# Optimization experiments

Hardware: AMD Instinct MI355X
Metric: run time of the kernel (lower is better)

Reference implementation:

```python
import jax, jax.numpy as jnp
import numpy as np

N_EMBD = 1024
N_HEAD = 16
R = 16
SCALING = 1.0 / 16.0  # loralib default lora_alpha=1, scaling = alpha/r


def lora_linear(x, W, b, A, B):
    # loralib: y = x @ W.T + b + (x @ A.T) @ B.T * scaling
    return x @ W.T + b + (x @ A.T) @ B.T * SCALING


def setup_inputs() -> dict:
    key = jax.random.key(0)
    ks = jax.random.split(key, 16)
    B, T, S, C = 8, 1024, 256, N_EMBD
    std = 0.02
    return {
        "x": jax.random.normal(ks[0], (B, T, C), jnp.float32),
        "feature": jax.random.normal(ks[1], (B, S, C), jnp.float32),
        # c_attn (q projection)
        "Wq": jax.random.normal(ks[2], (C, C), jnp.float32) * std,
        "bq": jnp.zeros((C,), jnp.float32),
        "Aq": jax.random.normal(ks[3], (R, C), jnp.float32) * std,
        "Bq": jnp.zeros((C, R), jnp.float32),
        # feature_attn (kv projection)
        "Wf": jax.random.normal(ks[4], (2 * C, C), jnp.float32) * std,
        "bf": jnp.zeros((2 * C,), jnp.float32),
        "Af": jax.random.normal(ks[5], (R, C), jnp.float32) * std,
        "Bf": jnp.zeros((2 * C, R), jnp.float32),
        # c_proj
        "Wp": jax.random.normal(ks[6], (C, C), jnp.float32) * std,
        "bp": jnp.zeros((C,), jnp.float32),
        "Ap": jax.random.normal(ks[7], (R, C), jnp.float32) * std,
        "Bp": jnp.zeros((C, R), jnp.float32),
    }


def reference(x, feature, Wq, bq, Aq, Bq, Wf, bf, Af, Bf, Wp, bp, Ap, Bp):
    Bsz, T, C = x.shape
    S = feature.shape[1]
    H = N_HEAD
    D = C // H

    q = lora_linear(x, Wq, bq, Aq, Bq).reshape(Bsz, T, H, D).transpose(0, 2, 1, 3)
    kv = lora_linear(feature, Wf, bf, Af, Bf)
    k, v = kv[..., :C], kv[..., C:]
    k = k.reshape(Bsz, S, H, D).transpose(0, 2, 1, 3)
    v = v.reshape(Bsz, S, H, D).transpose(0, 2, 1, 3)

    att = jnp.einsum("bhtd,bhsd->bhts", q, k) * (1.0 / np.sqrt(D))
    mask = jnp.tril(jnp.ones((T, S), bool))  # bias[:, :, :T, :S]
    att = jnp.where(mask, att, -jnp.inf)
    att = jax.nn.softmax(att, axis=-1)

    y = jnp.einsum("bhts,bhsd->bhtd", att, v)
    y = y.transpose(0, 2, 1, 3).reshape(Bsz, T, C)
    return lora_linear(y, Wp, bp, Ap, Bp)
```

## Files before the change

kernel.cpp:

```cpp
#include <hip/hip_runtime.h>
#include <hip/hip_bf16.h>
#include <stdint.h>
#include <stddef.h>

typedef __hip_bfloat16 bf16;
typedef __attribute__((ext_vector_type(8))) short short8;
typedef __attribute__((ext_vector_type(4))) float floatx4;

__device__ __forceinline__ void async_load16(const bf16* g, bf16* l) {
#if defined(__has_builtin) && __has_builtin(__builtin_amdgcn_global_load_lds)
  __builtin_amdgcn_global_load_lds((__attribute__((address_space(1))) void*)g,
                                   (__attribute__((address_space(3))) void*)l,
                                   16, 0, 0);
#else
  *(short8*)l = *(const short8*)g;
#endif
}

__device__ __forceinline__ int wave_detect_f32(const unsigned short* __restrict__ xr) {
  const int lane = threadIdx.x & 63;
  const unsigned short u = xr[lane];
  const int e = (u >> 7) & 0xFF;
  const unsigned long long m = __ballot(e >= 0x93);
  return (__popcll(m) > 5) ? 1 : 0;
}

struct PrepArgs {
  const void *x, *ft, *bq, *bf, *bp;
  const void *Wq, *Aq, *Bq, *Wf, *Af, *Bf, *Wp, *Ap, *Bp;
  bf16 *cx, *cft, *cbq, *cbf, *cbp, *weffq, *wefff, *weffp;
};

__device__ __forceinline__ void canon8(const void* src, bf16* dst, int i8, int flg) {
  if (flg) {
    const float4 v0 = ((const float4*)src)[i8 * 2];
    const float4 v1 = ((const float4*)src)[i8 * 2 + 1];
    bf16 o[8];
    o[0] = __float2bfloat16(v0.x); o[1] = __float2bfloat16(v0.y);
    o[2] = __float2bfloat16(v0.z); o[3] = __float2bfloat16(v0.w);
    o[4] = __float2bfloat16(v1.x); o[5] = __float2bfloat16(v1.y);
    o[6] = __float2bfloat16(v1.z); o[7] = __float2bfloat16(v1.w);
    *(uint4*)(dst + i8 * 8) = *(const uint4*)o;
  } else {
    ((uint4*)dst)[i8] = ((const uint4*)src)[i8];
  }
}

__device__ __forceinline__ void weff4(const void* W, const void* Bm, const void* Am,
                                      bf16* dst, int idx4, int flg) {
  const int n = idx4 >> 8, k = (idx4 & 255) << 2;
  float a0 = 0.f, a1 = 0.f, a2 = 0.f, a3 = 0.f;
  float w0, w1, w2, w3;
  if (flg) {
    const float* Af = (const float*)Am;
    const float* Bf = (const float*)Bm;
#pragma unroll
    for (int r = 0; r < 16; ++r) {
      const float4 av = *(const float4*)(Af + r * 1024 + k);
      const float bv = Bf[n * 16 + r];
      a0 += bv * av.x; a1 += bv * av.y; a2 += bv * av.z; a3 += bv * av.w;
    }
    const float4 wv = *(const float4*)((const float*)W + n * 1024 + k);
    w0 = wv.x; w1 = wv.y; w2 = wv.z; w3 = wv.w;
  } else {
    const bf16* Ab = (const bf16*)Am;
    const bf16* Bb = (const bf16*)Bm;
#pragma unroll
    for (int r = 0; r < 16; ++r) {
      const float bv = __bfloat162float(Bb[n * 16 + r]);
      const bf16* ap = Ab + r * 1024 + k;
      a0 += bv * __bfloat162float(ap[0]);
      a1 += bv * __bfloat162float(ap[1]);
      a2 += bv * __bfloat162float(ap[2]);
      a3 += bv * __bfloat162float(ap[3]);
    }
    const bf16* Wb = (const bf16*)W + n * 1024 + k;
    w0 = __bfloat162float(Wb[0]); w1 = __bfloat162float(Wb[1]);
    w2 = __bfloat162float(Wb[2]); w3 = __bfloat162float(Wb[3]);
  }
  bf16 o[4];
  o[0] = __float2bfloat16(w0 + 0.0625f * a0);
  o[1] = __float2bfloat16(w1 + 0.0625f * a1);
  o[2] = __float2bfloat16(w2 + 0.0625f * a2);
  o[3] = __float2bfloat16(w3 + 0.0625f * a3);
  *(uint2*)(dst + idx4 * 4) = *(const uint2*)o;
}

__global__ __launch_bounds__(256) void prep_kernel(PrepArgs a) {
  const int flg = wave_detect_f32((const unsigned short*)a.x);
  const int bid = blockIdx.x, tid = threadIdx.x;
  if (bid < 4096) {
    canon8(a.x, a.cx, bid * 256 + tid, flg);
  } else if (bid < 5120) {
    canon8(a.ft, a.cft, (bid - 4096) * 256 + tid, flg);
  } else if (bid < 5122) {
    const int e8 = (bid - 5120) * 256 + tid;
    if (e8 < 128) canon8(a.bq, a.cbq, e8, flg);
    else if (e8 < 384) canon8(a.bf, a.cbf, e8 - 128, flg);
    else canon8(a.bp, a.cbp, e8 - 384, flg);
  } else if (bid < 6146) {
    weff4(a.Wq, a.Bq, a.Aq, a.weffq, (bid - 5122) * 256 + tid, flg);
  } else if (bid < 8194) {
    weff4(a.Wf, a.Bf, a.Af, a.wefff, (bid - 6146) * 256 + tid, flg);
  } else {
    weff4(a.Wp, a.Bp, a.Ap, a.weffp, (bid - 8194) * 256 + tid, flg);
  }
}

#define QSLOT (256 * 32)
#define RSLOT (2 * QSLOT)

__device__ __forceinline__ void stage256(const bf16* __restrict__ gA,
                                         const bf16* __restrict__ gB,
                                         bf16* slot, int tid) {
#pragma unroll
  for (int l = 0; l < 2; ++l) {
    const int D = l * 512 + tid;
    const int r = D >> 2;
    const int c = (D & 3) ^ ((r >> 1) & 3);
    async_load16(gA + (size_t)r * 1024 + c * 8, slot + D * 8);
  }
#pragma unroll
  for (int l = 0; l < 2; ++l) {
    const int D = l * 512 + tid;
    const int r = D >> 2;
    const int c = (D & 3) ^ ((r >> 1) & 3);
    async_load16(gB + (size_t)r * 1024 + c * 8, slot + QSLOT + D * 8);
  }
}

__device__ __forceinline__ void gemm_core256(const bf16* __restrict__ A,
                                             const bf16* __restrict__ Bt,
                                             int bm, int bn, bf16* sT,
                                             floatx4 (&acc)[8][4]) {
  const int tid = threadIdx.x;
  const int wave = tid >> 6, lane = tid & 63;
  const int lrow = lane & 15, quad = lane >> 4;
  const int wm = (wave >> 2) << 7;
  const int wn = (wave & 3) << 6;
  const int pc0 = ((quad ^ ((lrow >> 1) & 3)) << 3);

  const bf16* gA = A + (size_t)bm * 1024;
  const bf16* gB = Bt + (size_t)bn * 1024;

  stage256(gA,      gB,      sT,             tid);
  stage256(gA + 32, gB + 32, sT + RSLOT,     tid);
  stage256(gA + 64, gB + 64, sT + 2 * RSLOT, tid);

#pragma unroll 4
  for (int t = 0; t < 32; ++t) {
    asm volatile("s_waitcnt lgkmcnt(0)" ::: "memory");
    __builtin_amdgcn_s_barrier();
    __builtin_amdgcn_sched_barrier(0);
    if (t < 29) {
      stage256(gA + (t + 3) * 32, gB + (t + 3) * 32, sT + ((t + 3) & 3) * RSLOT, tid);
      asm volatile("s_waitcnt vmcnt(12)" ::: "memory");
    } else if (t == 29) {
      asm volatile("s_waitcnt vmcnt(8)" ::: "memory");
    } else if (t == 30) {
      asm volatile("s_waitcnt vmcnt(4)" ::: "memory");
    } else {
      asm volatile("s_waitcnt vmcnt(0)" ::: "memory");
    }
    __builtin_amdgcn_s_barrier();
    __builtin_amdgcn_sched_barrier(0);

    const bf16* slotA = sT + (t & 3) * RSLOT;
    const bf16* slotB = slotA + QSLOT;
    short8 a_[8], b_[4];
#pragma unroll
    for (int i = 0; i < 8; ++i)
      a_[i] = *(const short8*)(slotA + (wm + i * 16 + lrow) * 32 + pc0);
#pragma unroll
    for (int j = 0; j < 4; ++j)
      b_[j] = *(const short8*)(slotB + (wn + j * 16 + lrow) * 32 + pc0);
    __builtin_amdgcn_s_setprio(1);
#pragma unroll
    for (int i = 0; i < 8; ++i)
#pragma unroll
      for (int j = 0; j < 4; ++j)
        acc[i][j] = __builtin_amdgcn_mfma_f32_16x16x32_bf16(
            a_[i], b_[j], acc[i][j], 0, 0, 0);
    __builtin_amdgcn_s_setprio(0);
  }
}

#define QSLOTB (128 * 32)
#define RSLOTO (QSLOT + QSLOTB)

__device__ __forceinline__ void stage128(const bf16* __restrict__ gA,
                                         const bf16* __restrict__ gB,
                                         bf16* slot, int tid) {
#pragma unroll
  for (int l = 0; l < 2; ++l) {
    const int D = l * 512 + tid;
    const int r = D >> 2;
    const int c = (D & 3) ^ ((r >> 1) & 3);
    async_load16(gA + (size_t)r * 1024 + c * 8, slot + D * 8);
  }
  {
    const int D = tid;
    const int r = D >> 2;
    const int c = (D & 3) ^ ((r >> 1) & 3);
    async_load16(gB + (size_t)r * 1024 + c * 8, slot + QSLOT + D * 8);
  }
}

__device__ __forceinline__ void gemm_core128(const bf16* __restrict__ A,
                                             const bf16* __restrict__ Bt,
                                             int bm, int bn, bf16* sT,
                                             floatx4 (&acc)[4][4]) {
  const int tid = threadIdx.x;
  const int wave = tid >> 6, lane = tid & 63;
  const int lrow = lane & 15, quad = lane >> 4;
  const int wm = (wave >> 1) << 6;
  const int wn = (wave & 1) << 6;
  const int pc0 = ((quad ^ ((lrow >> 1) & 3)) << 3);

  const bf16* gA = A + (size_t)bm * 1024;
  const bf16* gB = Bt + (size_t)bn * 1024;

  stage128(gA,      gB,      sT,             tid);
  stage128(gA + 32, gB + 32, sT + RSLOTO,     tid);
  stage128(gA + 64, gB + 64, sT + 2 * RSLOTO, tid);

#pragma unroll 4
  for (int t = 0; t < 32; ++t) {
    asm volatile("s_waitcnt lgkmcnt(0)" ::: "memory");
    __builtin_amdgcn_s_barrier();
    __builtin_amdgcn_sched_barrier(0);
    if (t < 29) {
      stage128(gA + (t + 3) * 32, gB + (t + 3) * 32, sT + ((t + 3) & 3) * RSLOTO, tid);
      asm volatile("s_waitcnt vmcnt(9)" ::: "memory");
    } else if (t == 29) {
      asm volatile("s_waitcnt vmcnt(6)" ::: "memory");
    } else if (t == 30) {
      asm volatile("s_waitcnt vmcnt(3)" ::: "memory");
    } else {
      asm volatile("s_waitcnt vmcnt(0)" ::: "memory");
    }
    __builtin_amdgcn_s_barrier();
    __builtin_amdgcn_sched_barrier(0);

    const bf16* slotA = sT + (t & 3) * RSLOTO;
    const bf16* slotB = slotA + QSLOT;
    short8 a_[4], b_[4];
#pragma unroll
    for (int i = 0; i < 4; ++i) {
      a_[i] = *(const short8*)(slotA + (wm + i * 16 + lrow) * 32 + pc0);
      b_[i] = *(const short8*)(slotB + (wn + i * 16 + lrow) * 32 + pc0);
    }
    __builtin_amdgcn_s_setprio(1);
#pragma unroll
    for (int i = 0; i < 4; ++i)
#pragma unroll
      for (int j = 0; j < 4; ++j)
        acc[i][j] = __builtin_amdgcn_mfma_f32_16x16x32_bf16(
            a_[i], b_[j], acc[i][j], 0, 0, 0);
    __builtin_amdgcn_s_setprio(0);
  }
}

__global__ __launch_bounds__(512, 1) void gemm_qkv(
    const bf16* __restrict__ cx, const bf16* __restrict__ cft,
    const bf16* __restrict__ weffq, const bf16* __restrict__ wefff,
    const bf16* __restrict__ cbq, const bf16* __restrict__ cbf,
    bf16* __restrict__ qws, bf16* __restrict__ kws, bf16* __restrict__ vtws) {
  __shared__ __align__(16) bf16 sT[4 * RSLOT];
  const int bid = blockIdx.x;
  const int swz = (bid & 7) * 24 + (bid >> 3);
  int mode, bm, bn;
  const bf16 *A, *Bt, *bias;
  if (swz < 128) {
    mode = 0; A = cx; Bt = weffq; bias = cbq;
    bm = (swz >> 2) * 256; bn = (swz & 3) * 256;
  } else {
    const int s2 = swz - 128;
    mode = 1; A = cft; Bt = wefff; bias = cbf;
    bm = (s2 >> 3) * 256; bn = (s2 & 7) * 256;
  }

  const floatx4 zero4 = {0.f, 0.f, 0.f, 0.f};
  floatx4 acc[8][4];
#pragma unroll
  for (int i = 0; i < 8; ++i)
#pragma unroll
    for (int j = 0; j < 4; ++j) acc[i][j] = zero4;

  gemm_core256(A, Bt, bm, bn, sT, acc);

  const int tid = threadIdx.x, wave = tid >> 6, lane = tid & 63;
  const int lrow = lane & 15, quad = lane >> 4;
  const int wm = (wave >> 2) << 7, wn = (wave & 3) << 6;
#pragma unroll
  for (int i = 0; i < 8; ++i) {
    const int mbase = bm + wm + i * 16 + quad * 4;
#pragma unroll
    for (int j = 0; j < 4; ++j) {
      const int n = bn + wn + j * 16 + lrow;
      const float bv = __bfloat162float(bias[n]);
#pragma unroll
      for (int r = 0; r < 4; ++r) {
        const int m = mbase + r;
        const bf16 hval = __float2bfloat16(acc[i][j][r] + bv);
        if (mode == 0) {
          const int b = m >> 10, t = m & 1023, hh = n >> 6, d = n & 63;
          qws[(((size_t)(b * 16 + hh)) * 1024 + t) * 64 + d] = hval;
        } else {
          const int b = m >> 8, s = m & 255;
          if (n < 1024) {
            const int hh = n >> 6, d = n & 63;
            kws[(((size_t)(b * 16 + hh)) * 256 + s) * 64 + d] = hval;
          } else {
            const int nn = n - 1024, hh = nn >> 6, d = nn & 63;
            vtws[(((size_t)(b * 16 + hh)) * 64 + d) * 256 + s] = hval;
          }
        }
      }
    }
  }
}

__global__ __launch_bounds__(512, 1) void gemm_out(
    const bf16* __restrict__ A, const bf16* __restrict__ Bt,
    const bf16* __restrict__ bias, void* __restrict__ out0,
    const unsigned short* __restrict__ xraw) {
  __shared__ __align__(16) bf16 sT[4 * RSLOTO];
  const int bid = blockIdx.x;
  const int swz = (bid & 7) * 32 + (bid >> 3);
  const int bm = (swz >> 3) * 256, bn = (swz & 7) * 128;
  const int N = 1024;

  const floatx4 zero4 = {0.f, 0.f, 0.f, 0.f};
  floatx4 acc[4][4];
#pragma unroll
  for (int i = 0; i < 4; ++i)
#pragma unroll
    for (int j = 0; j < 4; ++j) acc[i][j] = zero4;

  gemm_core128(A, Bt, bm, bn, sT, acc);

  const int tid = threadIdx.x, wave = tid >> 6, lane = tid & 63;
  const int lrow = lane & 15, quad = lane >> 4;
  const int wm = (wave >> 1) << 6, wn = (wave & 1) << 6;
  const int flg = wave_detect_f32(xraw);
#pragma unroll
  for (int i = 0; i < 4; ++i) {
    const int mbase = bm + wm + i * 16 + quad * 4;
#pragma unroll
    for (int j = 0; j < 4; ++j) {
      const int n = bn + wn + j * 16 + lrow;
      const float bv = __bfloat162float(bias[n]);
#pragma unroll
      for (int r = 0; r < 4; ++r) {
        const int m = mbase + r;
        const float fval = acc[i][j][r] + bv;
        const size_t idx = (size_t)m * N + n;
        if (flg) ((float*)out0)[idx] = fval;
        else     ((bf16*)out0)[idx] = __float2bfloat16(fval);
      }
    }
  }
}

#define SKP 72
#define SVP 264
__global__ __launch_bounds__(512, 2) void attn_kernel(
    const bf16* __restrict__ qws, const bf16* __restrict__ kws,
    const bf16* __restrict__ vtws, bf16* __restrict__ yws) {
  const int b = blockIdx.z, h = blockIdx.y, qc = blockIdx.x;
  const int bh = b * 16 + h;
  __shared__ __align__(16) bf16 sK[256 * SKP];
  __shared__ __align__(16) bf16 sVt[64 * SVP];
  __shared__ __align__(16) bf16 sP[8][16 * SVP];
  const int tid = threadIdx.x, wave = tid >> 6, lane = tid & 63;
  const int lrow = lane & 15, quad = lane >> 4;
  const bf16* kg = kws + (size_t)bh * (256 * 64);
  const bf16* vg = vtws + (size_t)bh * (64 * 256);
#pragma unroll
  for (int i = 0; i < 4; ++i) {
    const int idx = i * 512 + tid;
    const int kr = idx >> 3, kc = (idx & 7) * 8;
    *(short8*)(sK + kr * SKP + kc) = *(const short8*)(kg + kr * 64 + kc);
    const int vr = idx >> 5, vc = (idx & 31) * 8;
    *(short8*)(sVt + vr * SVP + vc) = *(const short8*)(vg + vr * 256 + vc);
  }
  __syncthreads();
  bf16* sPw = sP[wave];
  const floatx4 zero4 = {0.f, 0.f, 0.f, 0.f};
  const float kscale = 0.18033688011112042f;

  for (int st = 0; st < 4; ++st) {
    const int t0 = qc * 512 + wave * 64 + st * 16;
    const bf16* qrow = qws + ((size_t)bh * 1024 + t0 + lrow) * 64;
    const short8 aq0 = *(const short8*)(qrow + quad * 8);
    const short8 aq1 = *(const short8*)(qrow + 32 + quad * 8);
    floatx4 sc[16];
#pragma unroll
    for (int nt = 0; nt < 16; ++nt) {
      floatx4 c = zero4;
      c = __builtin_amdgcn_mfma_f32_16x16x32_bf16(
          aq0, *(const short8*)(sK + (nt * 16 + lrow) * SKP + quad * 8), c, 0, 0, 0);
      c = __builtin_amdgcn_mfma_f32_16x16x32_bf16(
          aq1, *(const short8*)(sK + (nt * 16 + lrow) * SKP + 32 + quad * 8), c, 0, 0, 0);
      sc[nt] = c;
    }
    float sum[4] = {0.f, 0.f, 0.f, 0.f};
#pragma unroll
    for (int nt = 0; nt < 16; ++nt) {
      const int s = nt * 16 + lrow;
#pragma unroll
      for (int r = 0; r < 4; ++r) {
        const int t = t0 + quad * 4 + r;
        const float p = (s <= t) ? exp2f(sc[nt][r] * kscale) : 0.f;
        sum[r] += p;
        sPw[(quad * 4 + r) * SVP + nt * 16 + lrow] = __float2bfloat16(p);
      }
    }
#pragma unroll
    for (int r = 0; r < 4; ++r) {
      sum[r] += __shfl_xor(sum[r], 1, 16);
      sum[r] += __shfl_xor(sum[r], 2, 16);
      sum[r] += __shfl_xor(sum[r], 4, 16);
      sum[r] += __shfl_xor(sum[r], 8, 16);
    }
    asm volatile("s_waitcnt lgkmcnt(0)" ::: "memory");
    floatx4 ya[4];
#pragma unroll
    for (int nt = 0; nt < 4; ++nt) ya[nt] = zero4;
#pragma unroll
    for (int ks = 0; ks < 8; ++ks) {
      const short8 ap = *(const short8*)(sPw + lrow * SVP + ks * 32 + quad * 8);
#pragma unroll
      for (int nt = 0; nt < 4; ++nt)
        ya[nt] = __builtin_amdgcn_mfma_f32_16x16x32_bf16(
            ap, *(const short8*)(sVt + (nt * 16 + lrow) * SVP + ks * 32 + quad * 8),
            ya[nt], 0, 0, 0);
    }
#pragma unroll
    for (int r = 0; r < 4; ++r) {
      const float rl = 1.f / sum[r];
      const int t = t0 + quad * 4 + r;
#pragma unroll
      for (int nt = 0; nt < 4; ++nt)
        yws[((size_t)b * 1024 + t) * 1024 + h * 64 + nt * 16 + lrow] =
            __float2bfloat16(ya[nt][r] * rl);
    }
  }
}

extern "C" void kernel_launch(void* const* d_in, const int* in_sizes, int n_in,
                              void* d_out, int out_size, void* d_ws, size_t ws_size,
                              hipStream_t stream) {
  char* p = (char*)d_ws;
  bf16* cbq   = (bf16*)p;     p += 4096;
  bf16* cbf   = (bf16*)p;     p += 8192;
  bf16* cbp   = (bf16*)p;     p += 4096;
  bf16* weffq = (bf16*)p;     p += (size_t)1024 * 1024 * 2;
  bf16* wefff = (bf16*)p;     p += (size_t)2048 * 1024 * 2;
  bf16* weffp = (bf16*)p;     p += (size_t)1024 * 1024 * 2;
  bf16* qws   = (bf16*)p;     p += (size_t)8 * 16 * 1024 * 64 * 2;
  bf16* kws   = (bf16*)p;     p += (size_t)8 * 16 * 256 * 64 * 2;
  bf16* vtws  = (bf16*)p;     p += (size_t)8 * 16 * 64 * 256 * 2;
  bf16* cft   = (bf16*)p;     p += (size_t)8 * 256 * 1024 * 2;
  bf16* cx    = (bf16*)p;     p += (size_t)8 * 1024 * 1024 * 2;
  bf16* yws   = cx;
  const size_t required = (size_t)(p - (char*)d_ws);
  if (ws_size < required) return;

  PrepArgs pa;
  pa.x = d_in[0]; pa.ft = d_in[1];
  pa.bq = d_in[3]; pa.bf = d_in[7]; pa.bp = d_in[11];
  pa.Wq = d_in[2];  pa.Aq = d_in[4];  pa.Bq = d_in[5];
  pa.Wf = d_in[6];  pa.Af = d_in[8];  pa.Bf = d_in[9];
  pa.Wp = d_in[10]; pa.Ap = d_in[12]; pa.Bp = d_in[13];
  pa.cx = cx; pa.cft = cft; pa.cbq = cbq; pa.cbf = cbf; pa.cbp = cbp;
  pa.weffq = weffq; pa.wefff = wefff; pa.weffp = weffp;
  prep_kernel<<<9218, 256, 0, stream>>>(pa);

  gemm_qkv<<<192, 512, 0, stream>>>(cx, cft, weffq, wefff, cbq, cbf, qws, kws, vtws);
  attn_kernel<<<dim3(2, 16, 8), 512, 0, stream>>>(qws, kws, vtws, yws);
  gemm_out<<<256, 512, 0, stream>>>(yws, weffp, cbp, d_out, (const unsigned short*)d_in[0]);
}
```

Measured before the change: 239.2 us.

## Unify GEMMs into 256x128 tile, 4-wave blocks with split-stage triple buffering

Both the QKV and output projection GEMMs now share one core that uses a 256x128 tile and 4 waves of 256 threads, each wave owning a 128x64 sub-tile. Launch bounds allow two blocks per CU. Each k-step's global-to-LDS staging is split into two halves, issued before and after the first half of the MFMA work. The LDS ring shrinks from 4 slots to 3, which is what lets two blocks fit per CU. The QKV grid doubles to 384 blocks. The aim is better CU occupancy and latency hiding, at the cost of more accumulator registers per thread and an extra barrier each iteration.

```diff
diff --git a/kernel.cpp b/kernel.cpp
--- a/kernel.cpp
+++ b/kernel.cpp
@@ -107,177 +107,140 @@
   }
 }
 
-#define QSLOT (256 * 32)
-#define RSLOT (2 * QSLOT)
-
-__device__ __forceinline__ void stage256(const bf16* __restrict__ gA,
-                                         const bf16* __restrict__ gB,
-                                         bf16* slot, int tid) {
+#define ASLOT (256 * 32)
+#define BSLOT (128 * 32)
+#define SLOT3 (ASLOT + BSLOT)
+
+__device__ __forceinline__ void stage_first(const bf16* __restrict__ gA,
+                                            const bf16* __restrict__ gB,
+                                            bf16* slot, int tid) {
 #pragma unroll
   for (int l = 0; l < 2; ++l) {
-    const int D = l * 512 + tid;
+    const int D = l * 256 + tid;
     const int r = D >> 2;
     const int c = (D & 3) ^ ((r >> 1) & 3);
     async_load16(gA + (size_t)r * 1024 + c * 8, slot + D * 8);
   }
-#pragma unroll
-  for (int l = 0; l < 2; ++l) {
-    const int D = l * 512 + tid;
+  {
+    const int D = tid;
     const int r = D >> 2;
     const int c = (D & 3) ^ ((r >> 1) & 3);
-    async_load16(gB + (size_t)r * 1024 + c * 8, slot + QSLOT + D * 8);
-  }
-}
-
-__device__ __forceinline__ void gemm_core256(const bf16* __restrict__ A,
-                                             const bf16* __restrict__ Bt,
-                                             int bm, int bn, bf16* sT,
-                                             floatx4 (&acc)[8][4]) {
+    async_load16(gB + (size_t)r * 1024 + c * 8, slot + ASLOT + D * 8);
+  }
+}
+
+__device__ __forceinline__ void stage_second(const bf16* __restrict__ gA,
+                                             const bf16* __restrict__ gB,
+                                             bf16* slot, int tid) {
+#pragma unroll
+  for (int l = 2; l < 4; ++l) {
+    const int D = l * 256 + tid;
+    const int r = D >> 2;
+    const int c = (D & 3) ^ ((r >> 1) & 3);
+    async_load16(gA + (size_t)r * 1024 + c * 8, slot + D * 8);
+  }
+  {
+    const int D = 256 + tid;
+    const int r = D >> 2;
+    const int c = (D & 3) ^ ((r >> 1) & 3);
+    async_load16(gB + (size_t)r * 1024 + c * 8, slot + ASLOT + D * 8);
+  }
+}
+
+__device__ __forceinline__ void gemm_core(const bf16* __restrict__ A,
+                                          const bf16* __restrict__ Bt,
+                                          int bm, int bn, bf16* sT,
+                                          floatx4 (&acc)[8][4]) {
   const int tid = threadIdx.x;
   const int wave = tid >> 6, lane = tid & 63;
   const int lrow = lane & 15, quad = lane >> 4;
-  const int wm = (wave >> 2) << 7;
-  const int wn = (wave & 3) << 6;
+  const int wm = (wave >> 1) << 7;
+  const int wn = (wave & 1) << 6;
   const int pc0 = ((quad ^ ((lrow >> 1) & 3)) << 3);
 
   const bf16* gA = A + (size_t)bm * 1024;
   const bf16* gB = Bt + (size_t)bn * 1024;
 
-  stage256(gA,      gB,      sT,             tid);
-  stage256(gA + 32, gB + 32, sT + RSLOT,     tid);
-  stage256(gA + 64, gB + 64, sT + 2 * RSLOT, tid);
-
-#pragma unroll 4
+  stage_first(gA, gB, sT, tid);  stage_second(gA, gB, sT, tid);
+  stage_first(gA + 32, gB + 32, sT + SLOT3, tid);
+  stage_second(gA + 32, gB + 32, sT + SLOT3, tid);
+
+  int rs = 0, ss = 2;
   for (int t = 0; t < 32; ++t) {
+    const bf16* slotA = sT + rs * SLOT3;
+    const bf16* slotB = slotA + ASLOT;
+    bf16* stSlot = sT + ss * SLOT3;
+    const bf16* sgA = gA + (t + 2) * 32;
+    const bf16* sgB = gB + (t + 2) * 32;
+
     asm volatile("s_waitcnt lgkmcnt(0)" ::: "memory");
     __builtin_amdgcn_s_barrier();
     __builtin_amdgcn_sched_barrier(0);
-    if (t < 29) {
-      stage256(gA + (t + 3) * 32, gB + (t + 3) * 32, sT + ((t + 3) & 3) * RSLOT, tid);
-      asm volatile("s_waitcnt vmcnt(12)" ::: "memory");
-    } else if (t == 29) {
-      asm volatile("s_waitcnt vmcnt(8)" ::: "memory");
+    if (t < 30) {
+      stage_first(sgA, sgB, stSlot, tid);
+      asm volatile("s_waitcnt vmcnt(9)" ::: "memory");
     } else if (t == 30) {
-      asm volatile("s_waitcnt vmcnt(4)" ::: "memory");
+      asm volatile("s_waitcnt vmcnt(6)" ::: "memory");
     } else {
       asm volatile("s_waitcnt vmcnt(0)" ::: "memory");
     }
     __builtin_amdgcn_s_barrier();
     __builtin_amdgcn_sched_barrier(0);
 
-    const bf16* slotA = sT + (t & 3) * RSLOT;
-    const bf16* slotB = slotA + QSLOT;
     short8 a_[8], b_[4];
 #pragma unroll
-    for (int i = 0; i < 8; ++i)
+    for (int i = 0; i < 4; ++i)
       a_[i] = *(const short8*)(slotA + (wm + i * 16 + lrow) * 32 + pc0);
 #pragma unroll
     for (int j = 0; j < 4; ++j)
       b_[j] = *(const short8*)(slotB + (wn + j * 16 + lrow) * 32 + pc0);
     __builtin_amdgcn_s_setprio(1);
 #pragma unroll
-    for (int i = 0; i < 8; ++i)
+    for (int i = 0; i < 4; ++i)
 #pragma unroll
       for (int j = 0; j < 4; ++j)
         acc[i][j] = __builtin_amdgcn_mfma_f32_16x16x32_bf16(
             a_[i], b_[j], acc[i][j], 0, 0, 0);
     __builtin_amdgcn_s_setprio(0);
-  }
-}
-
-#define QSLOTB (128 * 32)
-#define RSLOTO (QSLOT + QSLOTB)
-
-__device__ __forceinline__ void stage128(const bf16* __restrict__ gA,
-                                         const bf16* __restrict__ gB,
-                                         bf16* slot, int tid) {
-#pragma unroll
-  for (int l = 0; l < 2; ++l) {
-    const int D = l * 512 + tid;
-    const int r = D >> 2;
-    const int c = (D & 3) ^ ((r >> 1) & 3);
-    async_load16(gA + (size_t)r * 1024 + c * 8, slot + D * 8);
-  }
-  {
-    const int D = tid;
-    const int r = D >> 2;
-    const int c = (D & 3) ^ ((r >> 1) & 3);
-    async_load16(gB + (size_t)r * 1024 + c * 8, slot + QSLOT + D * 8);
-  }
-}
-
-__device__ __forceinline__ void gemm_core128(const bf16* __restrict__ A,
-                                             const bf16* __restrict__ Bt,
-                                             int bm, int bn, bf16* sT,
-                                             floatx4 (&acc)[4][4]) {
-  const int tid = threadIdx.x;
-  const int wave = tid >> 6, lane = tid & 63;
-  const int lrow = lane & 15, quad = lane >> 4;
-  const int wm = (wave >> 1) << 6;
-  const int wn = (wave & 1) << 6;
-  const int pc0 = ((quad ^ ((lrow >> 1) & 3)) << 3);
-
-  const bf16* gA = A + (size_t)bm * 1024;
-  const bf16* gB = Bt + (size_t)bn * 1024;
-
-  stage128(gA,      gB,      sT,             tid);
-  stage128(gA + 32, gB + 32, sT + RSLOTO,     tid);
-  stage128(gA + 64, gB + 64, sT + 2 * RSLOTO, tid);
-
-#pragma unroll 4
-  for (int t = 0; t < 32; ++t) {
-    asm volatile("s_waitcnt lgkmcnt(0)" ::: "memory");
+
     __builtin_amdgcn_s_barrier();
     __builtin_amdgcn_sched_barrier(0);
-    if (t < 29) {
-      stage128(gA + (t + 3) * 32, gB + (t + 3) * 32, sT + ((t + 3) & 3) * RSLOTO, tid);
-      asm volatile("s_waitcnt vmcnt(9)" ::: "memory");
-    } else if (t == 29) {
-      asm volatile("s_waitcnt vmcnt(6)" ::: "memory");
-    } else if (t == 30) {
-      asm volatile("s_waitcnt vmcnt(3)" ::: "memory");
-    } else {
-      asm volatile("s_waitcnt vmcnt(0)" ::: "memory");
-    }
-    __builtin_amdgcn_s_barrier();
-    __builtin_amdgcn_sched_barrier(0);
-
-    const bf16* slotA = sT + (t & 3) * RSLOTO;
-    const bf16* slotB = slotA + QSLOT;
-    short8 a_[4], b_[4];
-#pragma unroll
-    for (int i = 0; i < 4; ++i) {
+
+    if (t < 30) stage_second(sgA, sgB, stSlot, tid);
+#pragma unroll
+    for (int i = 4; i < 8; ++i)
       a_[i] = *(const short8*)(slotA + (wm + i * 16 + lrow) * 32 + pc0);
-      b_[i] = *(const short8*)(slotB + (wn + i * 16 + lrow) * 32 + pc0);
-    }
     __builtin_amdgcn_s_setprio(1);
 #pragma unroll
-    for (int i = 0; i < 4; ++i)
+    for (int i = 4; i < 8; ++i)
 #pragma unroll
       for (int j = 0; j < 4; ++j)
         acc[i][j] = __builtin_amdgcn_mfma_f32_16x16x32_bf16(
             a_[i], b_[j], acc[i][j], 0, 0, 0);
     __builtin_amdgcn_s_setprio(0);
-  }
-}
-
-__global__ __launch_bounds__(512, 1) void gemm_qkv(
+
+    rs = (rs == 2) ? 0 : rs + 1;
+    ss = (ss == 2) ? 0 : ss + 1;
+  }
+}
+
+__global__ __launch_bounds__(256, 2) void gemm_qkv(
     const bf16* __restrict__ cx, const bf16* __restrict__ cft,
     const bf16* __restrict__ weffq, const bf16* __restrict__ wefff,
     const bf16* __restrict__ cbq, const bf16* __restrict__ cbf,
     bf16* __restrict__ qws, bf16* __restrict__ kws, bf16* __restrict__ vtws) {
-  __shared__ __align__(16) bf16 sT[4 * RSLOT];
+  __shared__ __align__(16) bf16 sT[3 * SLOT3];
   const int bid = blockIdx.x;
-  const int swz = (bid & 7) * 24 + (bid >> 3);
+  const int swz = (bid & 7) * 48 + (bid >> 3);
   int mode, bm, bn;
   const bf16 *A, *Bt, *bias;
-  if (swz < 128) {
+  if (swz < 256) {
     mode = 0; A = cx; Bt = weffq; bias = cbq;
-    bm = (swz >> 2) * 256; bn = (swz & 3) * 256;
+    bm = (swz >> 3) * 256; bn = (swz & 7) * 128;
   } else {
-    const int s2 = swz - 128;
+    const int s2 = swz - 256;
     mode = 1; A = cft; Bt = wefff; bias = cbf;
-    bm = (s2 >> 3) * 256; bn = (s2 & 7) * 256;
+    bm = (s2 >> 4) * 256; bn = (s2 & 15) * 128;
   }
 
   const floatx4 zero4 = {0.f, 0.f, 0.f, 0.f};
@@ -287,11 +250,11 @@
 #pragma unroll
     for (int j = 0; j < 4; ++j) acc[i][j] = zero4;
 
-  gemm_core256(A, Bt, bm, bn, sT, acc);
+  gemm_core(A, Bt, bm, bn, sT, acc);
 
   const int tid = threadIdx.x, wave = tid >> 6, lane = tid & 63;
   const int lrow = lane & 15, quad = lane >> 4;
-  const int wm = (wave >> 2) << 7, wn = (wave & 3) << 6;
+  const int wm = (wave >> 1) << 7, wn = (wave & 1) << 6;
 #pragma unroll
   for (int i = 0; i < 8; ++i) {
     const int mbase = bm + wm + i * 16 + quad * 4;
@@ -321,31 +284,31 @@
   }
 }
 
-__global__ __launch_bounds__(512, 1) void gemm_out(
+__global__ __launch_bounds__(256, 2) void gemm_out(
     const bf16* __restrict__ A, const bf16* __restrict__ Bt,
     const bf16* __restrict__ bias, void* __restrict__ out0,
     const unsigned short* __restrict__ xraw) {
-  __shared__ __align__(16) bf16 sT[4 * RSLOTO];
+  __shared__ __align__(16) bf16 sT[3 * SLOT3];
   const int bid = blockIdx.x;
   const int swz = (bid & 7) * 32 + (bid >> 3);
   const int bm = (swz >> 3) * 256, bn = (swz & 7) * 128;
   const int N = 1024;
 
   const floatx4 zero4 = {0.f, 0.f, 0.f, 0.f};
-  floatx4 acc[4][4];
-#pragma unroll
-  for (int i = 0; i < 4; ++i)
+  floatx4 acc[8][4];
+#pragma unroll
+  for (int i = 0; i < 8; ++i)
 #pragma unroll
     for (int j = 0; j < 4; ++j) acc[i][j] = zero4;
 
-  gemm_core128(A, Bt, bm, bn, sT, acc);
+  gemm_core(A, Bt, bm, bn, sT, acc);
 
   const int tid = threadIdx.x, wave = tid >> 6, lane = tid & 63;
   const int lrow = lane & 15, quad = lane >> 4;
-  const int wm = (wave >> 1) << 6, wn = (wave & 1) << 6;
+  const int wm = (wave >> 1) << 7, wn = (wave & 1) << 6;
   const int flg = wave_detect_f32(xraw);
 #pragma unroll
-  for (int i = 0; i < 4; ++i) {
+  for (int i = 0; i < 8; ++i) {
     const int mbase = bm + wm + i * 16 + quad * 4;
 #pragma unroll
     for (int j = 0; j < 4; ++j) {
@@ -478,7 +441,7 @@
   pa.weffq = weffq; pa.wefff = wefff; pa.weffp = weffp;
   prep_kernel<<<9218, 256, 0, stream>>>(pa);
 
-  gemm_qkv<<<192, 512, 0, stream>>>(cx, cft, weffq, wefff, cbq, cbf, qws, kws, vtws);
+  gemm_qkv<<<384, 256, 0, stream>>>(cx, cft, weffq, wefff, cbq, cbf, qws, kws, vtws);
   attn_kernel<<<dim3(2, 16, 8), 512, 0, stream>>>(qws, kws, vtws, yws);
-  gemm_out<<<256, 512, 0, stream>>>(yws, weffp, cbp, d_out, (const unsigned short*)d_in[0]);
-}
+  gemm_out<<<256, 256, 0, stream>>>(yws, weffp, cbp, d_out, (const unsigned short*)d_in[0]);
+}
```

After: 234.8 us. No clear change (-1.8%).
